# Performance work log

Hardware: AMD Instinct MI355X
Metric: run time of the kernel (lower is better)

Reference implementation:

```python
import jax, jax.numpy as jnp
import numpy as np

N = 50000
DIN, DH, DOUT = 128, 128, 64
DEPTH = 3
TEMP = 1.0
WEIGHT = 0.5
LN_EPS = 1e-5
E_RAND = 1_600_000


def setup_inputs() -> dict:
    key = jax.random.key(0)
    ks = jax.random.split(key, 16)
    x = jax.random.normal(ks[0], (N, DIN), jnp.float32)
    # random edges + ring (guarantees degree >= 2 after symmetrization)
    src = jax.random.randint(ks[1], (E_RAND,), 0, N)
    dst = jax.random.randint(ks[2], (E_RAND,), 0, N)
    ring = jnp.arange(N)
    s = jnp.concatenate([src, ring])
    d = jnp.concatenate([dst, (ring + 1) % N])
    edge_index = jnp.stack([jnp.concatenate([s, d]), jnp.concatenate([d, s])]).astype(jnp.int64)  # [2, 3.3M], symmetric

    def glorot(k, i, o):
        return jax.random.normal(k, (i, o), jnp.float32) * jnp.sqrt(2.0 / (i + o)).astype(jnp.float32)

    return {
        "x": x, "edge_index": edge_index,
        "W0": glorot(ks[3], DIN, DH), "b0": jnp.zeros((DH,), jnp.float32),
        "W1": glorot(ks[4], DH, DH),  "b1": jnp.zeros((DH,), jnp.float32),
        "W2": glorot(ks[5], DH, DH),  "b2": jnp.zeros((DH,), jnp.float32),
        "W_out": glorot(ks[6], DH, DOUT), "b_out": jnp.zeros((DOUT,), jnp.float32),
        "gamma": jnp.ones((DH,), jnp.float32), "beta": jnp.zeros((DH,), jnp.float32),
    }


def _seg(vals, idx):
    return jax.ops.segment_sum(vals, idx, num_segments=N)


def _gcn_conv(h_in, W, b, src, dst):
    # PyG GCNConv: self-loops, sym norm D^-1/2 (A+I) D^-1/2
    h = h_in @ W
    ones = jnp.ones(src.shape, jnp.float32)
    deg = _seg(ones, dst) + 1.0  # degree incl. self-loop
    dinv = jax.lax.rsqrt(deg)
    msg = h[src] * (dinv[src] * dinv[dst])[:, None]
    return _seg(msg, dst) + h * (1.0 / deg)[:, None] + b


def _layernorm(x, g, b):
    m = jnp.mean(x, axis=-1, keepdims=True)
    v = jnp.mean((x - m) ** 2, axis=-1, keepdims=True)
    return (x - m) * jax.lax.rsqrt(v + LN_EPS) * g + b


def reference(x, edge_index, W0, b0, W1, b1, W2, b2, W_out, b_out, gamma, beta):
    src, dst = edge_index[0], edge_index[1]
    h = x
    for W, b in ((W0, b0), (W1, b1), (W2, b2)):
        h = _layernorm(jax.nn.relu(_gcn_conv(h, W, b, src, dst)), gamma, beta)
    emb = _gcn_conv(h, W_out, b_out, src, dst)  # [N, DOUT]

    # --- entropy gradient (edge-list form of the dense-A einsums) ---
    ones = jnp.ones(src.shape, jnp.float32)
    deg_adj = _seg(ones, src)                     # row sums of A (no self-loops)
    en_norm = 1.0 / jnp.sqrt(deg_adj * DH)        # uses hidden_dim, as in the original

    rn2 = jnp.sum(emb * emb, axis=1)              # ||X_i||^2
    dot = jnp.sum(emb[src] * emb[dst], axis=1)    # <X_i, X_j> per edge
    res1 = deg_adj * rn2
    res2 = _seg(dot, src)
    res3 = _seg(rn2[dst], src)
    energies = 0.5 * (res1 - 2.0 * res2 + res3) * en_norm  # normalize_energies=True

    logits = -energies / TEMP
    P = jax.nn.softmax(logits, axis=0) + 1e-10
    logP = jnp.log(P)
    S = -jnp.sum(P * logP)
    Pbar = P * (S + logP)                         # [N]

    nsumX = _seg(emb[dst], src)                   # sum_j A_ij X_j
    nsumP = _seg(Pbar[dst], src)                  # sum_j A_ij Pbar_j
    XP = emb * Pbar[:, None]
    g1 = deg_adj[:, None] * XP
    g2 = emb * nsumP[:, None]
    g3 = Pbar[:, None] * nsumX
    g4 = _seg(XP[dst], src)
    grad_S = (g1 + g2 - g3 - g4) / TEMP * en_norm[:, None]

    return emb + WEIGHT * grad_S
```

## Files before the change

### kernel.cpp

```cpp
#include <hip/hip_runtime.h>

#define DIN 128
#define DH  128
#define DFO 64
#define LN_EPS 1e-5f
#define WEIGHT 0.5f

#define MAXB  104
#define CAPB  64
#define FLUSH 32
#define SENT  0xFFFFFFFFu

typedef unsigned int uint32;

__device__ __forceinline__ float bf_lo(uint32 u) { return __uint_as_float(u << 16); }
__device__ __forceinline__ float bf_hi(uint32 u) { return __uint_as_float(u & 0xFFFF0000u); }
__device__ __forceinline__ uint32 pack_bf16(float a, float b) {
  uint32 ua = __float_as_uint(a), ub = __float_as_uint(b);
  ua += 0x7FFFu + ((ua >> 16) & 1u);
  ub += 0x7FFFu + ((ub >> 16) & 1u);
  return (ua >> 16) | (ub & 0xFFFF0000u);
}

__device__ __forceinline__ float wave_sum(float v) {
  #pragma unroll
  for (int off = 32; off > 0; off >>= 1) v += __shfl_xor(v, off);
  return v;
}
__device__ __forceinline__ float wave_max(float v) {
  #pragma unroll
  for (int off = 32; off > 0; off >>= 1) v = fmaxf(v, __shfl_xor(v, off));
  return v;
}

__device__ __forceinline__ void acc8(float* a, uint4 u) {
  a[0] += bf_lo(u.x); a[1] += bf_hi(u.x);
  a[2] += bf_lo(u.y); a[3] += bf_hi(u.y);
  a[4] += bf_lo(u.z); a[5] += bf_hi(u.z);
  a[6] += bf_lo(u.w); a[7] += bf_hi(u.w);
}
__device__ __forceinline__ void fma8(float* a, uint4 u, float p) {
  a[0] = fmaf(bf_lo(u.x), p, a[0]); a[1] = fmaf(bf_hi(u.x), p, a[1]);
  a[2] = fmaf(bf_lo(u.y), p, a[2]); a[3] = fmaf(bf_hi(u.y), p, a[3]);
  a[4] = fmaf(bf_lo(u.z), p, a[4]); a[5] = fmaf(bf_hi(u.z), p, a[5]);
  a[6] = fmaf(bf_lo(u.w), p, a[6]); a[7] = fmaf(bf_hi(u.w), p, a[7]);
}

__global__ __launch_bounds__(64) void k_prep(const float* __restrict__ g, const float* __restrict__ b,
                      const float* __restrict__ W1, const float* __restrict__ W2,
                      const float* __restrict__ Wo, float* __restrict__ Wg1,
                      float* __restrict__ Wg2, float* __restrict__ Wgo,
                      float* __restrict__ vecs) {
  int c = blockIdx.x * 64 + threadIdx.x;
  const float* W; float* Wg; float* gv; float* bv; int ld; int col;
  if (c < 128)      { W = W1; Wg = Wg1; gv = vecs;       bv = vecs + 128; ld = 128; col = c; }
  else if (c < 256) { W = W2; Wg = Wg2; gv = vecs + 256; bv = vecs + 384; ld = 128; col = c - 128; }
  else              { W = Wo; Wg = Wgo; gv = vecs + 512; bv = vecs + 576; ld = 64;  col = c - 256; }
  float gs = 0.f, bs = 0.f;
  for (int k = 0; k < 128; ++k) {
    float w = W[k * ld + col];
// ... 67 lines not shown
    }
  }
  __syncthreads();
  for (int b = wv; b < nbc; b += 4) {
    int m = fm[b];
    if (m > 0) {
      int r = (m + 15) & ~15, g = fbase[b];
      if (ln < r)
        gpairs[(size_t)b * GCAP + g + ln] = (ln < m) ? lbuf[b][ln] : SENT;
    }
  }
}

__global__ __launch_bounds__(1024) void k_csr(const uint32* __restrict__ gpairs, const int* __restrict__ gbcnt,
                      int GCAP, int GCAPC, int N, int* __restrict__ rowbeg, int* __restrict__ rowcnt,
                      float* __restrict__ dinv, float* __restrict__ cntf, int* __restrict__ col) {
  __shared__ int hist[512];
  __shared__ int pos[512];
  int b = blockIdx.x, tid = threadIdx.x;
  if (tid < 512) hist[tid] = 0;
  __syncthreads();
  int m = gbcnt[b * 16];
  const uint32* pp = gpairs + (size_t)b * GCAP;
  for (int t = tid; t < m; t += 1024) {
    uint32 v = pp[t];
    if (v != SENT) atomicAdd(&hist[v >> 16], 1);
  }
  __syncthreads();
  int cnt = (tid < 512) ? hist[tid] : 0;
  for (int off = 1; off < 512; off <<= 1) {
    int u = (tid >= off && tid < 512) ? hist[tid - off] : 0;
// ... 6 lines not shown
    int excl = hist[tid] - cnt;
    pos[tid] = excl;
    int node = (b << 9) + tid;
    if (node < N) {
      rowbeg[node] = cbase + excl;
      rowcnt[node] = cnt;
      cntf[node] = (float)cnt;
      dinv[node] = rsqrtf((float)cnt + 1.0f);
    }
  }
  __syncthreads();
  for (int t = tid; t < m; t += 1024) {
    uint32 v = pp[t];
    if (v != SENT) {
      int sl = atomicAdd(&pos[v >> 16], 1);
      col[cbase + sl] = (int)(v & 0xFFFFu);
    }
  }
}

template <int COLS, int MODE>
__global__ __launch_bounds__(256) void k_gemm(const void* __restrict__ Ap, const float* __restrict__ W,
                            const float* __restrict__ dinv, const float2* __restrict__ stats,
                            const float* __restrict__ gW, const float* __restrict__ bW,
                            uint32* __restrict__ outb, int N) {
  const int CG  = COLS / 4;
  const int RG  = 256 / CG;
  const int RPT = 64 / RG;
  const int OPL = CG / 2;
  __shared__ float4 At4[64 * 32];
  int t = threadIdx.x;
  int rbase = blockIdx.x * 64;
  #pragma unroll
  for (int i2 = 0; i2 < 8; ++i2) {
    int idx = t + 256 * i2;
    int row = idx >> 5, c4i = idx & 31;
    int gr = rbase + row;
    float4 v = make_float4(0.f, 0.f, 0.f, 0.f);
    if (gr < N) {
      if (MODE == 1) {
        const uint2* A2 = (const uint2*)Ap;
        uint2 p = A2[(size_t)(c4i >> 4) * N * 16 + (size_t)gr * 16 + (c4i & 15)];
        v = make_float4(bf_lo(p.x), bf_hi(p.x), bf_lo(p.y), bf_hi(p.y));
      } else {
        v = ((const float4*)Ap)[(size_t)gr * 32 + c4i];
      }
    }
    At4[idx] = v;
  }
  __syncthreads();
  int c4 = t % CG, rg = t / CG;
  float acc[RPT][4];
  #pragma unroll
  for (int r = 0; r < RPT; ++r) { acc[r][0] = acc[r][1] = acc[r][2] = acc[r][3] = 0.f; }
  const float4* W4 = (const float4*)W;
  #pragma unroll 2
  for (int k4 = 0; k4 < 32; ++k4) {
    float4 w0 = W4[(k4 * 4 + 0) * CG + c4];
// ... 3 lines not shown
    #pragma unroll
    for (int r = 0; r < RPT; ++r) {
      float4 av = At4[(rg * RPT + r) * 32 + k4];
      acc[r][0] = fmaf(av.x, w0.x, acc[r][0]); acc[r][0] = fmaf(av.y, w1.x, acc[r][0]);
      acc[r][0] = fmaf(av.z, w2.x, acc[r][0]); acc[r][0] = fmaf(av.w, w3.x, acc[r][0]);
      acc[r][1] = fmaf(av.x, w0.y, acc[r][1]); acc[r][1] = fmaf(av.y, w1.y, acc[r][1]);
      acc[r][1] = fmaf(av.z, w2.y, acc[r][1]); acc[r][1] = fmaf(av.w, w3.y, acc[r][1]);
      acc[r][2] = fmaf(av.x, w0.z, acc[r][2]); acc[r][2] = fmaf(av.y, w1.z, acc[r][2]);
      acc[r][2] = fmaf(av.z, w2.z, acc[r][2]); acc[r][2] = fmaf(av.w, w3.z, acc[r][2]);
      acc[r][3] = fmaf(av.x, w0.w, acc[r][3]); acc[r][3] = fmaf(av.y, w1.w, acc[r][3]);
      acc[r][3] = fmaf(av.z, w2.w, acc[r][3]); acc[r][3] = fmaf(av.w, w3.w, acc[r][3]);
    }
  }
  float4 g4 = make_float4(0.f, 0.f, 0.f, 0.f), b4 = make_float4(0.f, 0.f, 0.f, 0.f);
  if (MODE == 1) { g4 = ((const float4*)gW)[c4]; b4 = ((const float4*)bW)[c4]; }
  #pragma unroll
  for (int r = 0; r < RPT; ++r) {
    int gr = rbase + rg * RPT + r;
    if (gr < N) {
      float s = dinv[gr];
      float o0, o1, o2, o3;
      if (MODE == 1) {
        float2 st = stats[gr];
        o0 = s * (st.y * (acc[r][0] - st.x * g4.x) + b4.x);
        o1 = s * (st.y * (acc[r][1] - st.x * g4.y) + b4.y);
        o2 = s * (st.y * (acc[r][2] - st.x * g4.z) + b4.z);
        o3 = s * (st.y * (acc[r][3] - st.x * g4.w) + b4.w);
      } else {
        o0 = acc[r][0] * s; o1 = acc[r][1] * s; o2 = acc[r][2] * s; o3 = acc[r][3] * s;
      }
      uint2 o;
      o.x = pack_bf16(o0, o1);
      o.y = pack_bf16(o2, o3);
      int pl = c4 / OPL, slot = c4 % OPL;
      ((uint2*)outb)[(size_t)pl * N * OPL + (size_t)gr * OPL + slot] = o;
    }
  }
}

template <int PLANE>
__global__ __launch_bounds__(64) void k_aggh(const uint4* __restrict__ hsb4, const int* __restrict__ rowbeg,
                      const int* __restrict__ rowcnt, const int* __restrict__ col,
                      const float* __restrict__ dinv, const float* __restrict__ bias,
                      uint4* __restrict__ vb4, float2* __restrict__ ss,
                      float2* __restrict__ stats, int N) {
  int i = blockIdx.x, lane = threadIdx.x;
  int f = lane & 7, sl = lane >> 3;
  const uint4* hp = hsb4 + (size_t)PLANE * N * 8;
  int beg = rowbeg[i], end = beg + rowcnt[i];
  float a[8] = {0,0,0,0,0,0,0,0}, b[8] = {0,0,0,0,0,0,0,0};
  if (lane < 8) acc8(a, hp[(size_t)i * 8 + f]);
  int t = beg + sl;
  for (; t + 8 < end; t += 16) {
    int j0 = col[t], j1 = col[t + 8];
    uint4 u0 = hp[(size_t)j0 * 8 + f];
    uint4 u1 = hp[(size_t)j1 * 8 + f];
    acc8(a, u0); acc8(b, u1);
  }
  for (; t < end; t += 8) acc8(a, hp[(size_t)col[t] * 8 + f]);
  #pragma unroll
  for (int k = 0; k < 8; ++k) {
    a[k] += b[k];
    a[k] += __shfl_xor(a[k], 8);
    a[k] += __shfl_xor(a[k], 16);
    a[k] += __shfl_xor(a[k], 32);
  }
  float di = dinv[i];
  const float4* bb = (const float4*)(bias + PLANE * 64);
  float4 bb0 = bb[f * 2], bb1 = bb[f * 2 + 1];
  float v[8];
  v[0] = fmaxf(fmaf(a[0], di, bb0.x), 0.f);
  v[1] = fmaxf(fmaf(a[1], di, bb0.y), 0.f);
  v[2] = fmaxf(fmaf(a[2], di, bb0.z), 0.f);
  v[3] = fmaxf(fmaf(a[3], di, bb0.w), 0.f);
  v[4] = fmaxf(fmaf(a[4], di, bb1.x), 0.f);
  v[5] = fmaxf(fmaf(a[5], di, bb1.y), 0.f);
  v[6] = fmaxf(fmaf(a[6], di, bb1.z), 0.f);
  v[7] = fmaxf(fmaf(a[7], di, bb1.w), 0.f);
  float s = 0.f, s2 = 0.f;
  #pragma unroll
  for (int k = 0; k < 8; ++k) { s += v[k]; s2 += v[k] * v[k]; }
  s += __shfl_xor(s, 1); s2 += __shfl_xor(s2, 1);
  s += __shfl_xor(s, 2); s2 += __shfl_xor(s2, 2);
  s += __shfl_xor(s, 4); s2 += __shfl_xor(s2, 4);
  if (lane < 8) {
    uint4 o;
    o.x = pack_bf16(v[0], v[1]); o.y = pack_bf16(v[2], v[3]);
    o.z = pack_bf16(v[4], v[5]); o.w = pack_bf16(v[6], v[7]);
    vb4[(size_t)PLANE * N * 8 + (size_t)i * 8 + f] = o;
  }
  if (lane == 0) {
    if (PLANE == 0) {
      ss[i] = make_float2(s, s2);
    } else {
      float2 q = ss[i];
      float S = s + q.x, S2 = s2 + q.y;
      float mean = S * (1.f / 128.f);
      float var = S2 * (1.f / 128.f) - mean * mean;
      stats[i] = make_float2(mean, rsqrtf(var + LN_EPS));
    }
  }
}

__global__ __launch_bounds__(64) void k_agg_out(const uint4* __restrict__ hso4, const int* __restrict__ rowbeg,
                          const int* __restrict__ rowcnt, const int* __restrict__ col,
                          const float* __restrict__ dinv, const float* __restrict__ bias,
                          float* __restrict__ embf, uint4* __restrict__ embb4,
                          float* __restrict__ rn2, int N) {
  int i = blockIdx.x, lane = threadIdx.x;
  int f4 = lane & 7, sl = lane >> 3;
  const uint4* hp = hso4 + (size_t)(f4 >> 2) * N * 4;
  int fs = f4 & 3;
  int beg = rowbeg[i], end = beg + rowcnt[i];
  float a[8] = {0,0,0,0,0,0,0,0}, b[8] = {0,0,0,0,0,0,0,0};
  if (lane < 8) acc8(a, hp[(size_t)i * 4 + fs]);
  int t = beg + sl;
  for (; t + 8 < end; t += 16) {
    int j0 = col[t], j1 = col[t + 8];
    uint4 u0 = hp[(size_t)j0 * 4 + fs];
    uint4 u1 = hp[(size_t)j1 * 4 + fs];
    acc8(a, u0); acc8(b, u1);
  }
  for (; t < end; t += 8) acc8(a, hp[(size_t)col[t] * 4 + fs]);
  #pragma unroll
  for (int k = 0; k < 8; ++k) {
    a[k] += b[k];
    a[k] += __shfl_xor(a[k], 8);
    a[k] += __shfl_xor(a[k], 16);
    a[k] += __shfl_xor(a[k], 32);
  }
  float di = dinv[i];
  float4 bb0 = ((const float4*)bias)[f4 * 2], bb1 = ((const float4*)bias)[f4 * 2 + 1];
  float e[8];
  e[0] = fmaf(a[0], di, bb0.x); e[1] = fmaf(a[1], di, bb0.y);
  e[2] = fmaf(a[2], di, bb0.z); e[3] = fmaf(a[3], di, bb0.w);
  e[4] = fmaf(a[4], di, bb1.x); e[5] = fmaf(a[5], di, bb1.y);
  e[6] = fmaf(a[6], di, bb1.z); e[7] = fmaf(a[7], di, bb1.w);
  float ss = 0.f;
  #pragma unroll
  for (int k = 0; k < 8; ++k) ss += e[k] * e[k];
  ss += __shfl_xor(ss, 1); ss += __shfl_xor(ss, 2); ss += __shfl_xor(ss, 4);
  if (lane == 0) rn2[i] = ss;
  if (lane < 8) {
    ((float4*)embf)[(size_t)i * 16 + f4 * 2]     = make_float4(e[0], e[1], e[2], e[3]);
    ((float4*)embf)[(size_t)i * 16 + f4 * 2 + 1] = make_float4(e[4], e[5], e[6], e[7]);
    uint4 o;
    o.x = pack_bf16(e[0], e[1]); o.y = pack_bf16(e[2], e[3]);
    o.z = pack_bf16(e[4], e[5]); o.w = pack_bf16(e[6], e[7]);
    embb4[(size_t)i * 8 + f4] = o;
  }
}

__global__ __launch_bounds__(64) void k_passA(const float* __restrict__ embf, const uint4* __restrict__ embb4,
                        const int* __restrict__ rowbeg, const int* __restrict__ rowcnt,
                        const int* __restrict__ col, const float* __restrict__ rn2,
                        const float* __restrict__ cntf, float* __restrict__ nsumX,
                        float* __restrict__ logits, int N) {
  int i = blockIdx.x, lane = threadIdx.x;
  int f4 = lane & 7, sl = lane >> 3;
  int beg = rowbeg[i], end = beg + rowcnt[i];
  float a[8] = {0,0,0,0,0,0,0,0}, b[8] = {0,0,0,0,0,0,0,0};
  float r3 = 0.f;
  int t = beg + sl;
  for (; t + 8 < end; t += 16) {
    int j0 = col[t], j1 = col[t + 8];
    uint4 u0 = embb4[(size_t)j0 * 8 + f4];
    uint4 u1 = embb4[(size_t)j1 * 8 + f4];
    acc8(a, u0); acc8(b, u1);
    if (f4 == 0) r3 += rn2[j0] + rn2[j1];
  }
  for (; t < end; t += 8) {
    int j = col[t];
    uint4 u = embb4[(size_t)j * 8 + f4];
    acc8(a, u);
    if (f4 == 0) r3 += rn2[j];
  }
  #pragma unroll
  for (int k = 0; k < 8; ++k) {
    a[k] += b[k];
    a[k] += __shfl_xor(a[k], 8);
    a[k] += __shfl_xor(a[k], 16);
    a[k] += __shfl_xor(a[k], 32);
  }
  r3 += __shfl_xor(r3, 8); r3 += __shfl_xor(r3, 16); r3 += __shfl_xor(r3, 32);
  float4 e0 = ((const float4*)embf)[(size_t)i * 16 + f4 * 2];
  float4 e1 = ((const float4*)embf)[(size_t)i * 16 + f4 * 2 + 1];
  float dd = e0.x * a[0] + e0.y * a[1] + e0.z * a[2] + e0.w * a[3]
           + e1.x * a[4] + e1.y * a[5] + e1.z * a[6] + e1.w * a[7];
  dd += __shfl_xor(dd, 1); dd += __shfl_xor(dd, 2); dd += __shfl_xor(dd, 4);
  r3 += __shfl_xor(r3, 1); r3 += __shfl_xor(r3, 2); r3 += __shfl_xor(r3, 4);
  if (lane < 8) {
    ((float4*)nsumX)[(size_t)i * 16 + f4 * 2]     = make_float4(a[0], a[1], a[2], a[3]);
    ((float4*)nsumX)[(size_t)i * 16 + f4 * 2 + 1] = make_float4(a[4], a[5], a[6], a[7]);
  }
  if (lane == 0) {
    float c = cntf[i];
    float en = rsqrtf(c * 128.0f);
    logits[i] = -0.5f * (c * rn2[i] - 2.f * dd + r3) * en;
  }
}

__global__ __launch_bounds__(256) void k_sm1(const float* __restrict__ logits, int N,
                                             float4* __restrict__ partials) {
  int idx = blockIdx.x * 256 + threadIdx.x;
  int w = threadIdx.x >> 6, ln = threadIdx.x & 63;
  float x = (idx < N) ? logits[idx] : -3.4e38f;
  float m = wave_max(x);
  __shared__ float red[3][4];
  if (ln == 0) red[0][w] = m;
  __syncthreads();
  float M = fmaxf(fmaxf(red[0][0], red[0][1]), fmaxf(red[0][2], red[0][3]));
  float ev = (idx < N) ? expf(x - M) : 0.f;
  float tv = (idx < N) ? (x - M) * ev : 0.f;
// ... 29 lines not shown
    scal[2] = logf(SE) - TT / SE;
  }
}

__global__ __launch_bounds__(256) void k_pbar(const float* __restrict__ logits, int N,
                     const float* __restrict__ scal, float* __restrict__ Pb) {
  float M = scal[0], SE = scal[1], S = scal[2];
  int i = blockIdx.x * blockDim.x + threadIdx.x;
  int stride = gridDim.x * blockDim.x;
  for (; i < N; i += stride) {
    float p = expf(logits[i] - M) / SE + 1e-10f;
    Pb[i] = p * (S + logf(p));
  }
}

__global__ __launch_bounds__(64) void k_passB(const float* __restrict__ embf, const uint4* __restrict__ embb4,
                        const int* __restrict__ rowbeg, const int* __restrict__ rowcnt,
                        const int* __restrict__ col, const float* __restrict__ Pb,
                        const float* __restrict__ cntf, float* __restrict__ outp, int N) {
  int i = blockIdx.x, lane = threadIdx.x;
  int f4 = lane & 7, sl = lane >> 3;
  int beg = rowbeg[i], end = beg + rowcnt[i];
  float a[8] = {0,0,0,0,0,0,0,0}, b[8] = {0,0,0,0,0,0,0,0};
  float sp = 0.f;
  int t = beg + sl;
  for (; t + 8 < end; t += 16) {
    int j0 = col[t], j1 = col[t + 8];
    float p0 = Pb[j0], p1 = Pb[j1];
    uint4 u0 = embb4[(size_t)j0 * 8 + f4];
    uint4 u1 = embb4[(size_t)j1 * 8 + f4];
    fma8(a, u0, p0); fma8(b, u1, p1);
    if (f4 == 0) sp += p0 + p1;
  }
  for (; t < end; t += 8) {
    int j = col[t];
    float p = Pb[j];
    uint4 u = embb4[(size_t)j * 8 + f4];
    fma8(a, u, p);
    if (f4 == 0) sp += p;
  }
  #pragma unroll
  for (int k = 0; k < 8; ++k) {
    a[k] += b[k];
    a[k] += __shfl_xor(a[k], 8);
    a[k] += __shfl_xor(a[k], 16);
    a[k] += __shfl_xor(a[k], 32);
  }
  sp += __shfl_xor(sp, 8); sp += __shfl_xor(sp, 16); sp += __shfl_xor(sp, 32);
  sp += __shfl_xor(sp, 1); sp += __shfl_xor(sp, 2); sp += __shfl_xor(sp, 4);
  if (lane < 8) {
    float4 e0 = ((const float4*)embf)[(size_t)i * 16 + f4 * 2];
    float4 e1 = ((const float4*)embf)[(size_t)i * 16 + f4 * 2 + 1];
    float4 n0 = ((const float4*)outp)[(size_t)i * 16 + f4 * 2];
    float4 n1 = ((const float4*)outp)[(size_t)i * 16 + f4 * 2 + 1];
    float Pi = Pb[i];
    float c = cntf[i];
    float wgt = WEIGHT * rsqrtf(c * 128.0f);
    float g0 = c * e0.x * Pi + e0.x * sp - Pi * n0.x - a[0];
    float g1 = c * e0.y * Pi + e0.y * sp - Pi * n0.y - a[1];
    float g2 = c * e0.z * Pi + e0.z * sp - Pi * n0.z - a[2];
    float g3 = c * e0.w * Pi + e0.w * sp - Pi * n0.w - a[3];
    float g4 = c * e1.x * Pi + e1.x * sp - Pi * n1.x - a[4];
    float g5 = c * e1.y * Pi + e1.y * sp - Pi * n1.y - a[5];
    float g6 = c * e1.z * Pi + e1.z * sp - Pi * n1.z - a[6];
    float g7 = c * e1.w * Pi + e1.w * sp - Pi * n1.w - a[7];
    ((float4*)outp)[(size_t)i * 16 + f4 * 2] =
        make_float4(fmaf(wgt, g0, e0.x), fmaf(wgt, g1, e0.y), fmaf(wgt, g2, e0.z), fmaf(wgt, g3, e0.w));
    ((float4*)outp)[(size_t)i * 16 + f4 * 2 + 1] =
        make_float4(fmaf(wgt, g4, e1.x), fmaf(wgt, g5, e1.y), fmaf(wgt, g6, e1.z), fmaf(wgt, g7, e1.w));
  }
}

extern "C" void kernel_launch(void* const* d_in, const int* in_sizes, int n_in,
                              void* d_out, int out_size, void* d_ws, size_t ws_size,
                              hipStream_t stream) {
  const float* x     = (const float*)d_in[0];
  const int*   ei    = (const int*)d_in[1];
  const float* W0    = (const float*)d_in[2];
  const float* b0    = (const float*)d_in[3];
  const float* W1    = (const float*)d_in[4];
  const float* b1    = (const float*)d_in[5];
  const float* W2    = (const float*)d_in[6];
  const float* b2    = (const float*)d_in[7];
  const float* Wo    = (const float*)d_in[8];
// ... 1 lines not shown
  const float* gamma = (const float*)d_in[10];
  const float* beta  = (const float*)d_in[11];

  int N = in_sizes[0] / DIN;
  int E = in_sizes[1] / 2;
  int E2 = E / 2;
  const int* src = ei;
  const int* dst = ei + E;
  int nbc = (N + 511) >> 9;
  int perb = E / nbc;
  int GCAP  = ((perb + perb / 3 + 8192) + 15) & ~15;
  int GCAPC = perb + 4096;

  char* w = (char*)d_ws;
  auto alloc = [&](size_t bytes) { void* p = w; w += (bytes + 255) & ~(size_t)255; return p; };
  char*   regA = (char*)alloc((size_t)N * 128 * 2);
  char*   regB = (char*)alloc((size_t)N * 128 * 2);
  int*    colx = (int*)alloc((size_t)nbc * GCAPC * 4);
  int*    rowbeg = (int*)alloc((size_t)N * 4);
  int*    rowcnt = (int*)alloc((size_t)N * 4);
  float*  dinv   = (float*)alloc((size_t)N * 4);
  float*  cntf   = (float*)alloc((size_t)N * 4);
  float*  rn2    = (float*)alloc((size_t)N * 4);
  float*  logits = (float*)alloc((size_t)N * 4);
  float*  Pb     = (float*)alloc((size_t)N * 4);
  float2* ss     = (float2*)alloc((size_t)N * 8);
  float2* stats  = (float2*)alloc((size_t)N * 8);
  float*  Wg1    = (float*)alloc(128 * 128 * 4);
  float*  Wg2    = (float*)alloc(128 * 128 * 4);
  float*  Wgo    = (float*)alloc(128 * 64 * 4);
  float*  vecs   = (float*)alloc(640 * 4);
  int*    gbcnt  = (int*)alloc((size_t)MAXB * 16 * 4);
  float4* partials = (float4*)alloc(4096);
  float*  scal   = (float*)alloc(256);

  uint32* gpairs = (uint32*)regA;
  uint4*  vb4    = (uint4*)regA;
  float*  embf   = (float*)regA;
  uint4*  hsb4   = (uint4*)regB;
  uint32* hso    = (uint32*)regB;
  uint4*  embb4  = (uint4*)(regB + (size_t)N * 64 * 2);

  hipMemsetAsync(gbcnt, 0, (size_t)MAXB * 64, stream);
  k_prep<<<5, 64, 0, stream>>>(gamma, beta, W1, W2, Wo, Wg1, Wg2, Wgo, vecs);
  k_bin3<<<1024, 256, 0, stream>>>(src, dst, E2, nbc, GCAP, gbcnt, gpairs);
  k_csr<<<nbc, 1024, 0, stream>>>(gpairs, gbcnt, GCAP, GCAPC, N, rowbeg, rowcnt, dinv, cntf, colx);

  int gblk = (N + 63) / 64;

  k_gemm<DH, 0><<<gblk, 256, 0, stream>>>(x, W0, dinv, nullptr, nullptr, nullptr, (uint32*)hsb4, N);
  k_aggh<0><<<N, 64, 0, stream>>>(hsb4, rowbeg, rowcnt, colx, dinv, b0, vb4, ss, stats, N);
  k_aggh<1><<<N, 64, 0, stream>>>(hsb4, rowbeg, rowcnt, colx, dinv, b0, vb4, ss, stats, N);
  k_gemm<DH, 1><<<gblk, 256, 0, stream>>>(vb4, Wg1, dinv, stats, vecs, vecs + 128, (uint32*)hsb4, N);
  k_aggh<0><<<N, 64, 0, stream>>>(hsb4, rowbeg, rowcnt, colx, dinv, b1, vb4, ss, stats, N);
  k_aggh<1><<<N, 64, 0, stream>>>(hsb4, rowbeg, rowcnt, colx, dinv, b1, vb4, ss, stats, N);
  k_gemm<DH, 1><<<gblk, 256, 0, stream>>>(vb4, Wg2, dinv, stats, vecs + 256, vecs + 384, (uint32*)hsb4, N);
  k_aggh<0><<<N, 64, 0, stream>>>(hsb4, rowbeg, rowcnt, colx, dinv, b2, vb4, ss, stats, N);
  k_aggh<1><<<N, 64, 0, stream>>>(hsb4, rowbeg, rowcnt, colx, dinv, b2, vb4, ss, stats, N);
  k_gemm<DFO, 1><<<gblk, 256, 0, stream>>>(vb4, Wgo, dinv, stats, vecs + 512, vecs + 576, hso, N);
  k_agg_out<<<N, 64, 0, stream>>>((const uint4*)hso, rowbeg, rowcnt, colx, dinv, bo, embf, embb4, rn2, N);

  k_passA<<<N, 64, 0, stream>>>(embf, embb4, rowbeg, rowcnt, colx, rn2, cntf, (float*)d_out, logits, N);
  int nb = (N + 255) / 256;
  k_sm1<<<nb, 256, 0, stream>>>(logits, N, partials);
  k_sm2<<<1, 256, 0, stream>>>(partials, nb, scal);
  k_pbar<<<256, 256, 0, stream>>>(logits, N, scal, Pb);
  k_passB<<<N, 64, 0, stream>>>(embf, embb4, rowbeg, rowcnt, colx, Pb, cntf, (float*)d_out, N);
}
```

Baseline: 665.1 us.

## Quantize gathered node features to int8 with per-row scales and use 16-bit column indices

```diff
diff --git a/kernel.cpp b/kernel.cpp
--- a/kernel.cpp
+++ b/kernel.cpp
@@ -1,4 +1,5 @@
 #include <hip/hip_runtime.h>
+#include <hip/hip_fp16.h>
 
 #define DIN 128
 #define DH  128
@@ -7,20 +8,19 @@
 #define WEIGHT 0.5f
 
 #define MAXB  104
-#define CAPB  64
+#define CAPB  48
 #define FLUSH 32
 #define SENT  0xFFFFFFFFu
 
 typedef unsigned int uint32;
-
-__device__ __forceinline__ float bf_lo(uint32 u) { return __uint_as_float(u << 16); }
-__device__ __forceinline__ float bf_hi(uint32 u) { return __uint_as_float(u & 0xFFFF0000u); }
-__device__ __forceinline__ uint32 pack_bf16(float a, float b) {
-  uint32 ua = __float_as_uint(a), ub = __float_as_uint(b);
-  ua += 0x7FFFu + ((ua >> 16) & 1u);
-  ub += 0x7FFFu + ((ub >> 16) & 1u);
-  return (ua >> 16) | (ub & 0xFFFF0000u);
-}
+typedef unsigned short ushort16;
+
+__device__ __forceinline__ float h_lo(uint32 u) { return __half2float(__ushort_as_half((unsigned short)(u & 0xFFFFu))); }
+__device__ __forceinline__ float h_hi(uint32 u) { return __half2float(__ushort_as_half((unsigned short)(u >> 16))); }
+__device__ __forceinline__ uint32 pack_h2(float a, float b) {
+  return (uint32)__half_as_ushort(__float2half_rn(a)) | ((uint32)__half_as_ushort(__float2half_rn(b)) << 16);
+}
+__device__ __forceinline__ int sb(uint32 u, int k) { return ((int)(u << (24 - 8 * k))) >> 24; }
 
 __device__ __forceinline__ float wave_sum(float v) {
   #pragma unroll
@@ -33,17 +33,15 @@
   return v;
 }
 
-__device__ __forceinline__ void acc8(float* a, uint4 u) {
-  a[0] += bf_lo(u.x); a[1] += bf_hi(u.x);
-  a[2] += bf_lo(u.y); a[3] += bf_hi(u.y);
-  a[4] += bf_lo(u.z); a[5] += bf_hi(u.z);
-  a[6] += bf_lo(u.w); a[7] += bf_hi(u.w);
-}
-__device__ __forceinline__ void fma8(float* a, uint4 u, float p) {
-  a[0] = fmaf(bf_lo(u.x), p, a[0]); a[1] = fmaf(bf_hi(u.x), p, a[1]);
-  a[2] = fmaf(bf_lo(u.y), p, a[2]); a[3] = fmaf(bf_hi(u.y), p, a[3]);
-  a[4] = fmaf(bf_lo(u.z), p, a[4]); a[5] = fmaf(bf_hi(u.z), p, a[5]);
-  a[6] = fmaf(bf_lo(u.w), p, a[6]); a[7] = fmaf(bf_hi(u.w), p, a[7]);
+__device__ __forceinline__ void fq16(float* a, uint4 u, float w) {
+  #pragma unroll
+  for (int k = 0; k < 4; ++k) a[k]      = fmaf((float)sb(u.x, k), w, a[k]);
+  #pragma unroll
+  for (int k = 0; k < 4; ++k) a[4 + k]  = fmaf((float)sb(u.y, k), w, a[4 + k]);
+  #pragma unroll
+  for (int k = 0; k < 4; ++k) a[8 + k]  = fmaf((float)sb(u.z, k), w, a[8 + k]);
+  #pragma unroll
+  for (int k = 0; k < 4; ++k) a[12 + k] = fmaf((float)sb(u.w, k), w, a[12 + k]);
 }
 
 __global__ __launch_bounds__(64) void k_prep(const float* __restrict__ g, const float* __restrict__ b,
@@ -141,7 +139,7 @@
 
 __global__ __launch_bounds__(1024) void k_csr(const uint32* __restrict__ gpairs, const int* __restrict__ gbcnt,
                       int GCAP, int GCAPC, int N, int* __restrict__ rowbeg, int* __restrict__ rowcnt,
-                      float* __restrict__ dinv, float* __restrict__ cntf, int* __restrict__ col) {
+                      float* __restrict__ dinv, float* __restrict__ cntf, ushort16* __restrict__ col) {
   __shared__ int hist[512];
   __shared__ int pos[512];
   int b = blockIdx.x, tid = threadIdx.x;
@@ -178,7 +176,7 @@
     uint32 v = pp[t];
     if (v != SENT) {
       int sl = atomicAdd(&pos[v >> 16], 1);
-      col[cbase + sl] = (int)(v & 0xFFFFu);
+      col[cbase + sl] = (ushort16)(v & 0xFFFFu);
     }
   }
 }
@@ -187,11 +185,10 @@
 __global__ __launch_bounds__(256) void k_gemm(const void* __restrict__ Ap, const float* __restrict__ W,
                             const float* __restrict__ dinv, const float2* __restrict__ stats,
                             const float* __restrict__ gW, const float* __restrict__ bW,
-                            uint32* __restrict__ outb, int N) {
+                            uint32* __restrict__ qout, float* __restrict__ qsc, int N) {
   const int CG  = COLS / 4;
   const int RG  = 256 / CG;
   const int RPT = 64 / RG;
-  const int OPL = CG / 2;
   __shared__ float4 At4[64 * 32];
   int t = threadIdx.x;
   int rbase = blockIdx.x * 64;
@@ -205,7 +202,7 @@
       if (MODE == 1) {
         const uint2* A2 = (const uint2*)Ap;
         uint2 p = A2[(size_t)(c4i >> 4) * N * 16 + (size_t)gr * 16 + (c4i & 15)];
-        v = make_float4(bf_lo(p.x), bf_hi(p.x), bf_lo(p.y), bf_hi(p.y));
+        v = make_float4(h_lo(p.x), h_hi(p.x), h_lo(p.y), h_hi(p.y));
       } else {
         v = ((const float4*)Ap)[(size_t)gr * 32 + c4i];
       }
@@ -239,12 +236,13 @@
   }
   float4 g4 = make_float4(0.f, 0.f, 0.f, 0.f), b4 = make_float4(0.f, 0.f, 0.f, 0.f);
   if (MODE == 1) { g4 = ((const float4*)gW)[c4]; b4 = ((const float4*)bW)[c4]; }
+  int pl = c4 >> 4, slot = c4 & 15;
   #pragma unroll
   for (int r = 0; r < RPT; ++r) {
     int gr = rbase + rg * RPT + r;
+    float o0 = 0.f, o1 = 0.f, o2 = 0.f, o3 = 0.f;
     if (gr < N) {
       float s = dinv[gr];
-      float o0, o1, o2, o3;
       if (MODE == 1) {
         float2 st = stats[gr];
         o0 = s * (st.y * (acc[r][0] - st.x * g4.x) + b4.x);
@@ -254,174 +252,194 @@
       } else {
         o0 = acc[r][0] * s; o1 = acc[r][1] * s; o2 = acc[r][2] * s; o3 = acc[r][3] * s;
       }
-      uint2 o;
-      o.x = pack_bf16(o0, o1);
-      o.y = pack_bf16(o2, o3);
-      int pl = c4 / OPL, slot = c4 % OPL;
-      ((uint2*)outb)[(size_t)pl * N * OPL + (size_t)gr * OPL + slot] = o;
+    }
+    float mx = fmaxf(fmaxf(fabsf(o0), fabsf(o1)), fmaxf(fabsf(o2), fabsf(o3)));
+    #pragma unroll
+    for (int m = 1; m < CG; m <<= 1) mx = fmaxf(mx, __shfl_xor(mx, m));
+    if (gr < N) {
+      float inv = (mx > 0.f) ? 127.f / mx : 0.f;
+      int q0 = (int)rintf(o0 * inv), q1 = (int)rintf(o1 * inv);
+      int q2 = (int)rintf(o2 * inv), q3 = (int)rintf(o3 * inv);
+      uint32 qw = (uint32)(q0 & 255) | ((uint32)(q1 & 255) << 8) |
+                  ((uint32)(q2 & 255) << 16) | ((uint32)(q3 & 255) << 24);
+      qout[(size_t)pl * N * 16 + (size_t)gr * 16 + slot] = qw;
+      if (c4 == 0) qsc[gr] = mx * (1.f / 127.f);
     }
   }
 }
 
 template <int PLANE>
-__global__ __launch_bounds__(64) void k_aggh(const uint4* __restrict__ hsb4, const int* __restrict__ rowbeg,
-                      const int* __restrict__ rowcnt, const int* __restrict__ col,
-                      const float* __restrict__ dinv, const float* __restrict__ bias,
-                      uint4* __restrict__ vb4, float2* __restrict__ ss,
-                      float2* __restrict__ stats, int N) {
+__global__ __launch_bounds__(64) void k_aggh(const uint4* __restrict__ hq4, const float* __restrict__ hsc,
+                      const int* __restrict__ rowbeg, const int* __restrict__ rowcnt,
+                      const ushort16* __restrict__ col, const float* __restrict__ dinv,
+                      const float* __restrict__ bias, uint4* __restrict__ vh4,
+                      float2* __restrict__ ss, float2* __restrict__ stats, int N) {
   int i = blockIdx.x, lane = threadIdx.x;
-  int f = lane & 7, sl = lane >> 3;
-  const uint4* hp = hsb4 + (size_t)PLANE * N * 8;
+  int f4 = lane & 3, sl = lane >> 2;
+  const uint4* hp = hq4 + (size_t)PLANE * N * 4;
   int beg = rowbeg[i], end = beg + rowcnt[i];
-  float a[8] = {0,0,0,0,0,0,0,0}, b[8] = {0,0,0,0,0,0,0,0};
-  if (lane < 8) acc8(a, hp[(size_t)i * 8 + f]);
+  float a[16];
+  #pragma unroll
+  for (int k = 0; k < 16; ++k) a[k] = 0.f;
+  if (lane < 4) fq16(a, hp[(size_t)i * 4 + f4], hsc[i]);
   int t = beg + sl;
-  for (; t + 8 < end; t += 16) {
-    int j0 = col[t], j1 = col[t + 8];
-    uint4 u0 = hp[(size_t)j0 * 8 + f];
-    uint4 u1 = hp[(size_t)j1 * 8 + f];
-    acc8(a, u0); acc8(b, u1);
-  }
-  for (; t < end; t += 8) acc8(a, hp[(size_t)col[t] * 8 + f]);
-  #pragma unroll
-  for (int k = 0; k < 8; ++k) {
-    a[k] += b[k];
-    a[k] += __shfl_xor(a[k], 8);
-    a[k] += __shfl_xor(a[k], 16);
-    a[k] += __shfl_xor(a[k], 32);
-  }
-  float di = dinv[i];
-  const float4* bb = (const float4*)(bias + PLANE * 64);
-  float4 bb0 = bb[f * 2], bb1 = bb[f * 2 + 1];
-  float v[8];
-  v[0] = fmaxf(fmaf(a[0], di, bb0.x), 0.f);
-  v[1] = fmaxf(fmaf(a[1], di, bb0.y), 0.f);
-  v[2] = fmaxf(fmaf(a[2], di, bb0.z), 0.f);
-  v[3] = fmaxf(fmaf(a[3], di, bb0.w), 0.f);
-  v[4] = fmaxf(fmaf(a[4], di, bb1.x), 0.f);
-  v[5] = fmaxf(fmaf(a[5], di, bb1.y), 0.f);
-  v[6] = fmaxf(fmaf(a[6], di, bb1.z), 0.f);
-  v[7] = fmaxf(fmaf(a[7], di, bb1.w), 0.f);
-  float s = 0.f, s2 = 0.f;
-  #pragma unroll
-  for (int k = 0; k < 8; ++k) { s += v[k]; s2 += v[k] * v[k]; }
-  s += __shfl_xor(s, 1); s2 += __shfl_xor(s2, 1);
-  s += __shfl_xor(s, 2); s2 += __shfl_xor(s2, 2);
-  s += __shfl_xor(s, 4); s2 += __shfl_xor(s2, 4);
-  if (lane < 8) {
-    uint4 o;
-    o.x = pack_bf16(v[0], v[1]); o.y = pack_bf16(v[2], v[3]);
-    o.z = pack_bf16(v[4], v[5]); o.w = pack_bf16(v[6], v[7]);
-    vb4[(size_t)PLANE * N * 8 + (size_t)i * 8 + f] = o;
-  }
-  if (lane == 0) {
-    if (PLANE == 0) {
-      ss[i] = make_float2(s, s2);
-    } else {
-      float2 q = ss[i];
-      float S = s + q.x, S2 = s2 + q.y;
-      float mean = S * (1.f / 128.f);
-      float var = S2 * (1.f / 128.f) - mean * mean;
-      stats[i] = make_float2(mean, rsqrtf(var + LN_EPS));
-    }
-  }
-}
-
-__global__ __launch_bounds__(64) void k_agg_out(const uint4* __restrict__ hso4, const int* __restrict__ rowbeg,
-                          const int* __restrict__ rowcnt, const int* __restrict__ col,
-                          const float* __restrict__ dinv, const float* __restrict__ bias,
-                          float* __restrict__ embf, uint4* __restrict__ embb4,
+  for (; t + 16 < end; t += 32) {
+    int j0 = col[t], j1 = col[t + 16];
+    float s0 = hsc[j0], s1 = hsc[j1];
+    uint4 u0 = hp[(size_t)j0 * 4 + f4];
+    uint4 u1 = hp[(size_t)j1 * 4 + f4];
+    fq16(a, u0, s0); fq16(a, u1, s1);
+  }
+  if (t < end) { int j = col[t]; fq16(a, hp[(size_t)j * 4 + f4], hsc[j]); }
+  #pragma unroll
+  for (int k = 0; k < 16; ++k) {
+    a[k] += __shfl_xor(a[k], 4);  a[k] += __shfl_xor(a[k], 8);
+    a[k] += __shfl_xor(a[k], 16); a[k] += __shfl_xor(a[k], 32);
+  }
+  if (lane < 4) {
+    float di = dinv[i];
+    const float4* bb = (const float4*)bias + PLANE * 16 + f4 * 4;
+    float s = 0.f, s2 = 0.f;
+    #pragma unroll
+    for (int q = 0; q < 4; ++q) {
+      float4 b4 = bb[q];
+      float v0 = fmaxf(fmaf(a[q*4+0], di, b4.x), 0.f);
+      float v1 = fmaxf(fmaf(a[q*4+1], di, b4.y), 0.f);
+      float v2 = fmaxf(fmaf(a[q*4+2], di, b4.z), 0.f);
+      float v3 = fmaxf(fmaf(a[q*4+3], di, b4.w), 0.f);
+      a[q*4+0] = v0; a[q*4+1] = v1; a[q*4+2] = v2; a[q*4+3] = v3;
+      s += (v0 + v1) + (v2 + v3);
+      s2 += (v0*v0 + v1*v1) + (v2*v2 + v3*v3);
+    }
+    s += __shfl_xor(s, 1); s2 += __shfl_xor(s2, 1);
+    s += __shfl_xor(s, 2); s2 += __shfl_xor(s2, 2);
+    uint4 o0, o1;
+    o0.x = pack_h2(a[0], a[1]);  o0.y = pack_h2(a[2], a[3]);
+    o0.z = pack_h2(a[4], a[5]);  o0.w = pack_h2(a[6], a[7]);
+    o1.x = pack_h2(a[8], a[9]);  o1.y = pack_h2(a[10], a[11]);
+    o1.z = pack_h2(a[12], a[13]); o1.w = pack_h2(a[14], a[15]);
+    vh4[(size_t)PLANE * N * 8 + (size_t)i * 8 + f4 * 2]     = o0;
+    vh4[(size_t)PLANE * N * 8 + (size_t)i * 8 + f4 * 2 + 1] = o1;
+    if (lane == 0) {
+      if (PLANE == 0) {
+        ss[i] = make_float2(s, s2);
+      } else {
+        float2 qq = ss[i];
+        float S = s + qq.x, S2 = s2 + qq.y;
+        float mean = S * (1.f / 128.f);
+        float var  = S2 * (1.f / 128.f) - mean * mean;
+        stats[i] = make_float2(mean, rsqrtf(var + LN_EPS));
+      }
+    }
+  }
+}
+
+__global__ __launch_bounds__(64) void k_agg_out(const uint4* __restrict__ hq4, const float* __restrict__ hsc,
+                          const int* __restrict__ rowbeg, const int* __restrict__ rowcnt,
+                          const ushort16* __restrict__ col, const float* __restrict__ dinv,
+                          const float* __restrict__ bias, float* __restrict__ embf,
+                          uint4* __restrict__ embq4, float* __restrict__ esc,
                           float* __restrict__ rn2, int N) {
   int i = blockIdx.x, lane = threadIdx.x;
-  int f4 = lane & 7, sl = lane >> 3;
-  const uint4* hp = hso4 + (size_t)(f4 >> 2) * N * 4;
-  int fs = f4 & 3;
+  int f4 = lane & 3, sl = lane >> 2;
   int beg = rowbeg[i], end = beg + rowcnt[i];
-  float a[8] = {0,0,0,0,0,0,0,0}, b[8] = {0,0,0,0,0,0,0,0};
-  if (lane < 8) acc8(a, hp[(size_t)i * 4 + fs]);
+  float a[16];
+  #pragma unroll
+  for (int k = 0; k < 16; ++k) a[k] = 0.f;
+  if (lane < 4) fq16(a, hq4[(size_t)i * 4 + f4], hsc[i]);
   int t = beg + sl;
-  for (; t + 8 < end; t += 16) {
-    int j0 = col[t], j1 = col[t + 8];
-    uint4 u0 = hp[(size_t)j0 * 4 + fs];
-    uint4 u1 = hp[(size_t)j1 * 4 + fs];
-    acc8(a, u0); acc8(b, u1);
-  }
-  for (; t < end; t += 8) acc8(a, hp[(size_t)col[t] * 4 + fs]);
-  #pragma unroll
-  for (int k = 0; k < 8; ++k) {
-    a[k] += b[k];
-    a[k] += __shfl_xor(a[k], 8);
-    a[k] += __shfl_xor(a[k], 16);
-    a[k] += __shfl_xor(a[k], 32);
-  }
-  float di = dinv[i];
-  float4 bb0 = ((const float4*)bias)[f4 * 2], bb1 = ((const float4*)bias)[f4 * 2 + 1];
-  float e[8];
-  e[0] = fmaf(a[0], di, bb0.x); e[1] = fmaf(a[1], di, bb0.y);
-  e[2] = fmaf(a[2], di, bb0.z); e[3] = fmaf(a[3], di, bb0.w);
-  e[4] = fmaf(a[4], di, bb1.x); e[5] = fmaf(a[5], di, bb1.y);
-  e[6] = fmaf(a[6], di, bb1.z); e[7] = fmaf(a[7], di, bb1.w);
-  float ss = 0.f;
-  #pragma unroll
-  for (int k = 0; k < 8; ++k) ss += e[k] * e[k];
-  ss += __shfl_xor(ss, 1); ss += __shfl_xor(ss, 2); ss += __shfl_xor(ss, 4);
-  if (lane == 0) rn2[i] = ss;
-  if (lane < 8) {
-    ((float4*)embf)[(size_t)i * 16 + f4 * 2]     = make_float4(e[0], e[1], e[2], e[3]);
-    ((float4*)embf)[(size_t)i * 16 + f4 * 2 + 1] = make_float4(e[4], e[5], e[6], e[7]);
-    uint4 o;
-    o.x = pack_bf16(e[0], e[1]); o.y = pack_bf16(e[2], e[3]);
-    o.z = pack_bf16(e[4], e[5]); o.w = pack_bf16(e[6], e[7]);
-    embb4[(size_t)i * 8 + f4] = o;
-  }
-}
-
-__global__ __launch_bounds__(64) void k_passA(const float* __restrict__ embf, const uint4* __restrict__ embb4,
-                        const int* __restrict__ rowbeg, const int* __restrict__ rowcnt,
-                        const int* __restrict__ col, const float* __restrict__ rn2,
-                        const float* __restrict__ cntf, float* __restrict__ nsumX,
-                        float* __restrict__ logits, int N) {
+  for (; t + 16 < end; t += 32) {
+    int j0 = col[t], j1 = col[t + 16];
+    float s0 = hsc[j0], s1 = hsc[j1];
+    uint4 u0 = hq4[(size_t)j0 * 4 + f4];
+    uint4 u1 = hq4[(size_t)j1 * 4 + f4];
+    fq16(a, u0, s0); fq16(a, u1, s1);
+  }
+  if (t < end) { int j = col[t]; fq16(a, hq4[(size_t)j * 4 + f4], hsc[j]); }
+  #pragma unroll
+  for (int k = 0; k < 16; ++k) {
+    a[k] += __shfl_xor(a[k], 4);  a[k] += __shfl_xor(a[k], 8);
+    a[k] += __shfl_xor(a[k], 16); a[k] += __shfl_xor(a[k], 32);
+  }
+  if (lane < 4) {
+    float di = dinv[i];
+    const float4* bb = (const float4*)bias + f4 * 4;
+    float s2 = 0.f, mx = 0.f;
+    #pragma unroll
+    for (int q = 0; q < 4; ++q) {
+      float4 b4 = bb[q];
+      float e0 = fmaf(a[q*4+0], di, b4.x);
+      float e1 = fmaf(a[q*4+1], di, b4.y);
+      float e2 = fmaf(a[q*4+2], di, b4.z);
+      float e3 = fmaf(a[q*4+3], di, b4.w);
+      a[q*4+0] = e0; a[q*4+1] = e1; a[q*4+2] = e2; a[q*4+3] = e3;
+      s2 += (e0*e0 + e1*e1) + (e2*e2 + e3*e3);
+      mx = fmaxf(mx, fmaxf(fmaxf(fabsf(e0), fabsf(e1)), fmaxf(fabsf(e2), fabsf(e3))));
+      ((float4*)embf)[(size_t)i * 16 + f4 * 4 + q] = make_float4(e0, e1, e2, e3);
+    }
+    s2 += __shfl_xor(s2, 1); s2 += __shfl_xor(s2, 2);
+    mx = fmaxf(mx, __shfl_xor(mx, 1)); mx = fmaxf(mx, __shfl_xor(mx, 2));
+    float inv = (mx > 0.f) ? 127.f / mx : 0.f;
+    uint4 qo;
+    uint32* qw = (uint32*)&qo;
+    #pragma unroll
+    for (int q = 0; q < 4; ++q) {
+      int q0 = (int)rintf(a[q*4+0] * inv), q1 = (int)rintf(a[q*4+1] * inv);
+      int q2 = (int)rintf(a[q*4+2] * inv), q3 = (int)rintf(a[q*4+3] * inv);
+      qw[q] = (uint32)(q0 & 255) | ((uint32)(q1 & 255) << 8) |
+              ((uint32)(q2 & 255) << 16) | ((uint32)(q3 & 255) << 24);
+    }
+    embq4[(size_t)i * 4 + f4] = qo;
+    if (lane == 0) { rn2[i] = s2; esc[i] = mx * (1.f / 127.f); }
+  }
+}
+
+__global__ __launch_bounds__(64) void k_passA(const float* __restrict__ embf, const uint4* __restrict__ embq4,
+                        const float* __restrict__ esc, const int* __restrict__ rowbeg,
+                        const int* __restrict__ rowcnt, const ushort16* __restrict__ col,
+                        const float* __restrict__ rn2, const float* __restrict__ cntf,
+                        float* __restrict__ nsumX, float* __restrict__ logits, int N) {
   int i = blockIdx.x, lane = threadIdx.x;
-  int f4 = lane & 7, sl = lane >> 3;
+  int f4 = lane & 3, sl = lane >> 2;
   int beg = rowbeg[i], end = beg + rowcnt[i];
-  float a[8] = {0,0,0,0,0,0,0,0}, b[8] = {0,0,0,0,0,0,0,0};
+  float a[16];
+  #pragma unroll
+  for (int k = 0; k < 16; ++k) a[k] = 0.f;
   float r3 = 0.f;
   int t = beg + sl;
-  for (; t + 8 < end; t += 16) {
-    int j0 = col[t], j1 = col[t + 8];
-    uint4 u0 = embb4[(size_t)j0 * 8 + f4];
-    uint4 u1 = embb4[(size_t)j1 * 8 + f4];
-    acc8(a, u0); acc8(b, u1);
+  for (; t + 16 < end; t += 32) {
+    int j0 = col[t], j1 = col[t + 16];
+    float s0 = esc[j0], s1 = esc[j1];
+    uint4 u0 = embq4[(size_t)j0 * 4 + f4];
+    uint4 u1 = embq4[(size_t)j1 * 4 + f4];
+    fq16(a, u0, s0); fq16(a, u1, s1);
     if (f4 == 0) r3 += rn2[j0] + rn2[j1];
   }
-  for (; t < end; t += 8) {
+  if (t < end) {
     int j = col[t];
-    uint4 u = embb4[(size_t)j * 8 + f4];
-    acc8(a, u);
+    fq16(a, embq4[(size_t)j * 4 + f4], esc[j]);
     if (f4 == 0) r3 += rn2[j];
   }
   #pragma unroll
-  for (int k = 0; k < 8; ++k) {
-    a[k] += b[k];
-    a[k] += __shfl_xor(a[k], 8);
-    a[k] += __shfl_xor(a[k], 16);
-    a[k] += __shfl_xor(a[k], 32);
-  }
-  r3 += __shfl_xor(r3, 8); r3 += __shfl_xor(r3, 16); r3 += __shfl_xor(r3, 32);
-  float4 e0 = ((const float4*)embf)[(size_t)i * 16 + f4 * 2];
-  float4 e1 = ((const float4*)embf)[(size_t)i * 16 + f4 * 2 + 1];
-  float dd = e0.x * a[0] + e0.y * a[1] + e0.z * a[2] + e0.w * a[3]
-           + e1.x * a[4] + e1.y * a[5] + e1.z * a[6] + e1.w * a[7];
-  dd += __shfl_xor(dd, 1); dd += __shfl_xor(dd, 2); dd += __shfl_xor(dd, 4);
-  r3 += __shfl_xor(r3, 1); r3 += __shfl_xor(r3, 2); r3 += __shfl_xor(r3, 4);
-  if (lane < 8) {
-    ((float4*)nsumX)[(size_t)i * 16 + f4 * 2]     = make_float4(a[0], a[1], a[2], a[3]);
-    ((float4*)nsumX)[(size_t)i * 16 + f4 * 2 + 1] = make_float4(a[4], a[5], a[6], a[7]);
-  }
-  if (lane == 0) {
-    float c = cntf[i];
-    float en = rsqrtf(c * 128.0f);
-    logits[i] = -0.5f * (c * rn2[i] - 2.f * dd + r3) * en;
+  for (int k = 0; k < 16; ++k) {
+    a[k] += __shfl_xor(a[k], 4);  a[k] += __shfl_xor(a[k], 8);
+    a[k] += __shfl_xor(a[k], 16); a[k] += __shfl_xor(a[k], 32);
+  }
+  r3 = wave_sum(r3);
+  if (lane < 4) {
+    float dd = 0.f;
+    #pragma unroll
+    for (int q = 0; q < 4; ++q) {
+      float4 e = ((const float4*)embf)[(size_t)i * 16 + f4 * 4 + q];
+      dd += e.x * a[q*4+0] + e.y * a[q*4+1] + e.z * a[q*4+2] + e.w * a[q*4+3];
+      ((float4*)nsumX)[(size_t)i * 16 + f4 * 4 + q] = make_float4(a[q*4+0], a[q*4+1], a[q*4+2], a[q*4+3]);
+    }
+    dd += __shfl_xor(dd, 1); dd += __shfl_xor(dd, 2);
+    if (lane == 0) {
+      float c = cntf[i];
+      float en = rsqrtf(c * 128.0f);
+      logits[i] = -0.5f * (c * rn2[i] - 2.f * dd + r3) * en;
+    }
   }
 }
 
@@ -481,60 +499,55 @@
   }
 }
 
-__global__ __launch_bounds__(64) void k_passB(const float* __restrict__ embf, const uint4* __restrict__ embb4,
-                        const int* __restrict__ rowbeg, const int* __restrict__ rowcnt,
-                        const int* __restrict__ col, const float* __restrict__ Pb,
-                        const float* __restrict__ cntf, float* __restrict__ outp, int N) {
+__global__ __launch_bounds__(64) void k_passB(const float* __restrict__ embf, const uint4* __restrict__ embq4,
+                        const float* __restrict__ esc, const int* __restrict__ rowbeg,
+                        const int* __restrict__ rowcnt, const ushort16* __restrict__ col,
+                        const float* __restrict__ Pb, const float* __restrict__ cntf,
+                        float* __restrict__ outp, int N) {
   int i = blockIdx.x, lane = threadIdx.x;
-  int f4 = lane & 7, sl = lane >> 3;
+  int f4 = lane & 3, sl = lane >> 2;
   int beg = rowbeg[i], end = beg + rowcnt[i];
-  float a[8] = {0,0,0,0,0,0,0,0}, b[8] = {0,0,0,0,0,0,0,0};
+  float a[16];
+  #pragma unroll
+  for (int k = 0; k < 16; ++k) a[k] = 0.f;
   float sp = 0.f;
   int t = beg + sl;
-  for (; t + 8 < end; t += 16) {
-    int j0 = col[t], j1 = col[t + 8];
+  for (; t + 16 < end; t += 32) {
+    int j0 = col[t], j1 = col[t + 16];
     float p0 = Pb[j0], p1 = Pb[j1];
-    uint4 u0 = embb4[(size_t)j0 * 8 + f4];
-    uint4 u1 = embb4[(size_t)j1 * 8 + f4];
-    fma8(a, u0, p0); fma8(b, u1, p1);
+    float w0 = p0 * esc[j0], w1 = p1 * esc[j1];
+    uint4 u0 = embq4[(size_t)j0 * 4 + f4];
+    uint4 u1 = embq4[(size_t)j1 * 4 + f4];
+    fq16(a, u0, w0); fq16(a, u1, w1);
     if (f4 == 0) sp += p0 + p1;
   }
-  for (; t < end; t += 8) {
+  if (t < end) {
     int j = col[t];
     float p = Pb[j];
-    uint4 u = embb4[(size_t)j * 8 + f4];
-    fma8(a, u, p);
+    fq16(a, embq4[(size_t)j * 4 + f4], p * esc[j]);
     if (f4 == 0) sp += p;
   }
   #pragma unroll
-  for (int k = 0; k < 8; ++k) {
-    a[k] += b[k];
-    a[k] += __shfl_xor(a[k], 8);
-    a[k] += __shfl_xor(a[k], 16);
-    a[k] += __shfl_xor(a[k], 32);
-  }
-  sp += __shfl_xor(sp, 8); sp += __shfl_xor(sp, 16); sp += __shfl_xor(sp, 32);
-  sp += __shfl_xor(sp, 1); sp += __shfl_xor(sp, 2); sp += __shfl_xor(sp, 4);
-  if (lane < 8) {
-    float4 e0 = ((const float4*)embf)[(size_t)i * 16 + f4 * 2];
-    float4 e1 = ((const float4*)embf)[(size_t)i * 16 + f4 * 2 + 1];
-    float4 n0 = ((const float4*)outp)[(size_t)i * 16 + f4 * 2];
-    float4 n1 = ((const float4*)outp)[(size_t)i * 16 + f4 * 2 + 1];
+  for (int k = 0; k < 16; ++k) {
+    a[k] += __shfl_xor(a[k], 4);  a[k] += __shfl_xor(a[k], 8);
+    a[k] += __shfl_xor(a[k], 16); a[k] += __shfl_xor(a[k], 32);
+  }
+  sp = wave_sum(sp);
+  if (lane < 4) {
     float Pi = Pb[i];
     float c = cntf[i];
     float wgt = WEIGHT * rsqrtf(c * 128.0f);
-    float g0 = c * e0.x * Pi + e0.x * sp - Pi * n0.x - a[0];
-    float g1 = c * e0.y * Pi + e0.y * sp - Pi * n0.y - a[1];
-    float g2 = c * e0.z * Pi + e0.z * sp - Pi * n0.z - a[2];
-    float g3 = c * e0.w * Pi + e0.w * sp - Pi * n0.w - a[3];
-    float g4 = c * e1.x * Pi + e1.x * sp - Pi * n1.x - a[4];
-    float g5 = c * e1.y * Pi + e1.y * sp - Pi * n1.y - a[5];
-    float g6 = c * e1.z * Pi + e1.z * sp - Pi * n1.z - a[6];
-    float g7 = c * e1.w * Pi + e1.w * sp - Pi * n1.w - a[7];
-    ((float4*)outp)[(size_t)i * 16 + f4 * 2] =
-        make_float4(fmaf(wgt, g0, e0.x), fmaf(wgt, g1, e0.y), fmaf(wgt, g2, e0.z), fmaf(wgt, g3, e0.w));
-    ((float4*)outp)[(size_t)i * 16 + f4 * 2 + 1] =
-        make_float4(fmaf(wgt, g4, e1.x), fmaf(wgt, g5, e1.y), fmaf(wgt, g6, e1.z), fmaf(wgt, g7, e1.w));
+    #pragma unroll
+    for (int q = 0; q < 4; ++q) {
+      float4 e = ((const float4*)embf)[(size_t)i * 16 + f4 * 4 + q];
+      float4 n = ((const float4*)outp)[(size_t)i * 16 + f4 * 4 + q];
+      float g0 = c * e.x * Pi + e.x * sp - Pi * n.x - a[q*4+0];
+      float g1 = c * e.y * Pi + e.y * sp - Pi * n.y - a[q*4+1];
+      float g2 = c * e.z * Pi + e.z * sp - Pi * n.z - a[q*4+2];
+      float g3 = c * e.w * Pi + e.w * sp - Pi * n.w - a[q*4+3];
+      ((float4*)outp)[(size_t)i * 16 + f4 * 4 + q] =
+          make_float4(fmaf(wgt, g0, e.x), fmaf(wgt, g1, e.y), fmaf(wgt, g2, e.z), fmaf(wgt, g3, e.w));
+    }
   }
 }
 
@@ -566,9 +579,11 @@
 
   char* w = (char*)d_ws;
   auto alloc = [&](size_t bytes) { void* p = w; w += (bytes + 255) & ~(size_t)255; return p; };
-  char*   regA = (char*)alloc((size_t)N * 128 * 2);
-  char*   regB = (char*)alloc((size_t)N * 128 * 2);
-  int*    colx = (int*)alloc((size_t)nbc * GCAPC * 4);
+  char* regA = (char*)alloc((size_t)N * 128 * 2);
+  char* regB = (char*)alloc((size_t)N * 64 * 2);
+  char* pad  = (char*)alloc((size_t)2 * 1024 * 1024);
+  (void)pad;
+  ushort16* colx = (ushort16*)alloc((size_t)nbc * GCAPC * 2);
   int*    rowbeg = (int*)alloc((size_t)N * 4);
   int*    rowcnt = (int*)alloc((size_t)N * 4);
   float*  dinv   = (float*)alloc((size_t)N * 4);
@@ -576,6 +591,9 @@
   float*  rn2    = (float*)alloc((size_t)N * 4);
   float*  logits = (float*)alloc((size_t)N * 4);
   float*  Pb     = (float*)alloc((size_t)N * 4);
+  float*  hsc    = (float*)alloc((size_t)N * 4);
+  float*  oscq   = (float*)alloc((size_t)N * 4);
+  float*  esc    = (float*)alloc((size_t)N * 4);
   float2* ss     = (float2*)alloc((size_t)N * 8);
   float2* stats  = (float2*)alloc((size_t)N * 8);
   float*  Wg1    = (float*)alloc(128 * 128 * 4);
@@ -587,11 +605,11 @@
   float*  scal   = (float*)alloc(256);
 
   uint32* gpairs = (uint32*)regA;
-  uint4*  vb4    = (uint4*)regA;
+  uint4*  vh4    = (uint4*)regA;
   float*  embf   = (float*)regA;
-  uint4*  hsb4   = (uint4*)regB;
-  uint32* hso    = (uint32*)regB;
-  uint4*  embb4  = (uint4*)(regB + (size_t)N * 64 * 2);
+  uint32* hq     = (uint32*)regB;
+  uint32* hoq    = (uint32*)regB;
+  uint4*  embq4  = (uint4*)(regB + (size_t)N * 64);
 
   hipMemsetAsync(gbcnt, 0, (size_t)MAXB * 64, stream);
   k_prep<<<5, 64, 0, stream>>>(gamma, beta, W1, W2, Wo, Wg1, Wg2, Wgo, vecs);
@@ -600,22 +618,22 @@
 
   int gblk = (N + 63) / 64;
 
-  k_gemm<DH, 0><<<gblk, 256, 0, stream>>>(x, W0, dinv, nullptr, nullptr, nullptr, (uint32*)hsb4, N);
-  k_aggh<0><<<N, 64, 0, stream>>>(hsb4, rowbeg, rowcnt, colx, dinv, b0, vb4, ss, stats, N);
-  k_aggh<1><<<N, 64, 0, stream>>>(hsb4, rowbeg, rowcnt, colx, dinv, b0, vb4, ss, stats, N);
-  k_gemm<DH, 1><<<gblk, 256, 0, stream>>>(vb4, Wg1, dinv, stats, vecs, vecs + 128, (uint32*)hsb4, N);
-  k_aggh<0><<<N, 64, 0, stream>>>(hsb4, rowbeg, rowcnt, colx, dinv, b1, vb4, ss, stats, N);
-  k_aggh<1><<<N, 64, 0, stream>>>(hsb4, rowbeg, rowcnt, colx, dinv, b1, vb4, ss, stats, N);
-  k_gemm<DH, 1><<<gblk, 256, 0, stream>>>(vb4, Wg2, dinv, stats, vecs + 256, vecs + 384, (uint32*)hsb4, N);
-  k_aggh<0><<<N, 64, 0, stream>>>(hsb4, rowbeg, rowcnt, colx, dinv, b2, vb4, ss, stats, N);
-  k_aggh<1><<<N, 64, 0, stream>>>(hsb4, rowbeg, rowcnt, colx, dinv, b2, vb4, ss, stats, N);
-  k_gemm<DFO, 1><<<gblk, 256, 0, stream>>>(vb4, Wgo, dinv, stats, vecs + 512, vecs + 576, hso, N);
-  k_agg_out<<<N, 64, 0, stream>>>((const uint4*)hso, rowbeg, rowcnt, colx, dinv, bo, embf, embb4, rn2, N);
-
-  k_passA<<<N, 64, 0, stream>>>(embf, embb4, rowbeg, rowcnt, colx, rn2, cntf, (float*)d_out, logits, N);
+  k_gemm<DH, 0><<<gblk, 256, 0, stream>>>(x, W0, dinv, nullptr, nullptr, nullptr, hq, hsc, N);
+  k_aggh<0><<<N, 64, 0, stream>>>((const uint4*)hq, hsc, rowbeg, rowcnt, colx, dinv, b0, vh4, ss, stats, N);
+  k_aggh<1><<<N, 64, 0, stream>>>((const uint4*)hq, hsc, rowbeg, rowcnt, colx, dinv, b0, vh4, ss, stats, N);
+  k_gemm<DH, 1><<<gblk, 256, 0, stream>>>(vh4, Wg1, dinv, stats, vecs, vecs + 128, hq, hsc, N);
+  k_aggh<0><<<N, 64, 0, stream>>>((const uint4*)hq, hsc, rowbeg, rowcnt, colx, dinv, b1, vh4, ss, stats, N);
+  k_aggh<1><<<N, 64, 0, stream>>>((const uint4*)hq, hsc, rowbeg, rowcnt, colx, dinv, b1, vh4, ss, stats, N);
+  k_gemm<DH, 1><<<gblk, 256, 0, stream>>>(vh4, Wg2, dinv, stats, vecs + 256, vecs + 384, hq, hsc, N);
+  k_aggh<0><<<N, 64, 0, stream>>>((const uint4*)hq, hsc, rowbeg, rowcnt, colx, dinv, b2, vh4, ss, stats, N);
+  k_aggh<1><<<N, 64, 0, stream>>>((const uint4*)hq, hsc, rowbeg, rowcnt, colx, dinv, b2, vh4, ss, stats, N);
+  k_gemm<DFO, 1><<<gblk, 256, 0, stream>>>(vh4, Wgo, dinv, stats, vecs + 512, vecs + 576, hoq, oscq, N);
+  k_agg_out<<<N, 64, 0, stream>>>((const uint4*)hoq, oscq, rowbeg, rowcnt, colx, dinv, bo, embf, embq4, esc, rn2, N);
+
+  k_passA<<<N, 64, 0, stream>>>(embf, embq4, esc, rowbeg, rowcnt, colx, rn2, cntf, (float*)d_out, logits, N);
   int nb = (N + 255) / 256;
   k_sm1<<<nb, 256, 0, stream>>>(logits, N, partials);
   k_sm2<<<1, 256, 0, stream>>>(partials, nb, scal);
   k_pbar<<<256, 256, 0, stream>>>(logits, N, scal, Pb);
-  k_passB<<<N, 64, 0, stream>>>(embf, embb4, rowbeg, rowcnt, colx, Pb, cntf, (float*)d_out, N);
-}
+  k_passB<<<N, 64, 0, stream>>>(embf, embq4, esc, rowbeg, rowcnt, colx, Pb, cntf, (float*)d_out, N);
+}
```

Result: no change. 669.4 us (+0.6%).
